# Performance work log

Hardware: AMD Instinct MI355X
Metric: run time of the kernel (lower is better)

## Reference

```python
import jax, jax.numpy as jnp
import numpy as np

N_NODES = 100000
N_EDGES = 3200000
FEAT_DIM = 128
EMBED_DIM = 128


def setup_inputs() -> dict:
    key = jax.random.key(0)
    k1, k2, k3, k4, k5 = jax.random.split(key, 5)
    x = jax.random.normal(k1, (N_NODES, FEAT_DIM), dtype=jnp.float32)
    weight = jax.random.normal(k2, (EMBED_DIM, FEAT_DIM), dtype=jnp.float32) * (1.0 / np.sqrt(FEAT_DIM))
    edge_weight = jax.random.uniform(k3, (N_EDGES,), dtype=jnp.float32)
    edge_src = jax.random.randint(k4, (N_EDGES,), 0, N_NODES, dtype=jnp.int32)
    edge_dst = jnp.sort(jax.random.randint(k5, (N_EDGES,), 0, N_NODES, dtype=jnp.int32))
    return {"x": x, "weight": weight, "edge_weight": edge_weight,
            "edge_src": edge_src, "edge_dst": edge_dst}


def reference(x, weight, edge_weight, edge_src, edge_dst):
    # Unfused GCN layer: dense transform then sparse aggregation.
    # h = X W^T  : [N, embed_dim]
    h = jnp.einsum('nf,ef->ne', x, weight)
    # out = A @ h, with A given as weighted edge list (dst <- src).
    msgs = edge_weight[:, None] * h[edge_src]          # [E, embed_dim]
    out = jax.ops.segment_sum(msgs, edge_dst, num_segments=N_NODES)
    return out
```

## Files before the change

kernel.cpp:

```cpp
#include <hip/hip_runtime.h>

#define NN 100000
#define NE 3200000
#define FEAT 128
#define EMBED 128

typedef __attribute__((ext_vector_type(8))) __bf16 bf16x8;
typedef __attribute__((ext_vector_type(8))) unsigned short ushort8;
typedef __attribute__((ext_vector_type(4))) float f32x4;

static __device__ __forceinline__ unsigned short f2bf(float f) {
    unsigned u = __float_as_uint(f);
    return (unsigned short)((u + 0x7FFFu + ((u >> 16) & 1u)) >> 16);
}

__global__ void convert_w(const float* __restrict__ w, unsigned short* __restrict__ wbf) {
    int i = blockIdx.x * 256 + threadIdx.x;
    if (i < EMBED * FEAT) wbf[i] = f2bf(w[i]);
}

__global__ __launch_bounds__(256)
void gemm_xwT(const float* __restrict__ x, const unsigned short* __restrict__ wbf,
              unsigned short* __restrict__ hbf) {
    int wave = blockIdx.x * 4 + (threadIdx.x >> 6);
    long row0 = (long)wave * 16;
    if (row0 >= NN) return;
    int lane = threadIdx.x & 63;
    int r = lane & 15, kg = lane >> 4;

    const float4* x4 = (const float4*)x;
    const bf16x8* wb = (const bf16x8*)wbf;

    bf16x8 afr[4];
#pragma unroll
    for (int ks = 0; ks < 4; ++ks) {
        long base = (row0 + r) * 32 + ks * 8 + kg * 2;
        float4 v0 = x4[base];
        float4 v1 = x4[base + 1];
        float xf[8] = {v0.x, v0.y, v0.z, v0.w, v1.x, v1.y, v1.z, v1.w};
        ushort8 au;
#pragma unroll
        for (int e = 0; e < 8; ++e) au[e] = f2bf(xf[e]);
        afr[ks] = __builtin_bit_cast(bf16x8, au);
    }

    f32x4 acc[8];
#pragma unroll
    for (int nt = 0; nt < 8; ++nt) acc[nt] = (f32x4){0.f, 0.f, 0.f, 0.f};

#pragma unroll
    for (int nt = 0; nt < 8; ++nt) {
#pragma unroll
        for (int ks = 0; ks < 4; ++ks) {
            bf16x8 b = wb[(nt * 16 + r) * 16 + ks * 4 + kg];
            acc[nt] = __builtin_amdgcn_mfma_f32_16x16x32_bf16(afr[ks], b, acc[nt], 0, 0, 0);
        }
    }

#pragma unroll
    for (int nt = 0; nt < 8; ++nt) {
#pragma unroll
        for (int reg = 0; reg < 4; ++reg) {
            hbf[(row0 + kg * 4 + reg) * 128 + nt * 16 + r] = f2bf(acc[nt][reg]);
        }
    }
}

__global__ void build_rowptr(const int* __restrict__ dst, int* __restrict__ rowptr) {
    int n = blockIdx.x * blockDim.x + threadIdx.x;
    if (n > NN) return;
    int lo = 0, hi = NE;
    while (lo < hi) {
        int mid = (lo + hi) >> 1;
        if (dst[mid] < n) lo = mid + 1; else hi = mid;
    }
    rowptr[n] = lo;
}

#define CONS(vj, wjv)                                                         \
    acc[0] += wjv * __uint_as_float(vj.x << 16);                              \
    acc[1] += wjv * __uint_as_float(vj.x & 0xFFFF0000u);                      \
    acc[2] += wjv * __uint_as_float(vj.y << 16);                              \
    acc[3] += wjv * __uint_as_float(vj.y & 0xFFFF0000u);                      \
    acc[4] += wjv * __uint_as_float(vj.z << 16);                              \
    acc[5] += wjv * __uint_as_float(vj.z & 0xFFFF0000u);                      \
    acc[6] += wjv * __uint_as_float(vj.w << 16);                              \
    acc[7] += wjv * __uint_as_float(vj.w & 0xFFFF0000u);

__global__ __launch_bounds__(256)
void aggregate(const unsigned int* __restrict__ h32, const float* __restrict__ ew,
               const int* __restrict__ src, const int* __restrict__ rowptr,
               float* __restrict__ out) {
    int wave = (int)((blockIdx.x * 256u + threadIdx.x) >> 6);
    int lane = threadIdx.x & 63;
    int nid0 = wave * 8;
    if (nid0 >= NN) return;

    int q = lane >> 4;
    int c = lane & 15;
    const uint4* h4 = (const uint4*)h32;

    int start = __builtin_amdgcn_readfirstlane(rowptr[nid0]);
    int nmax = NN - nid0 < 8 ? NN - nid0 : 8;

    for (int k = 0; k < nmax; ++k) {
        int nid = nid0 + k;
        int end = __builtin_amdgcn_readfirstlane(rowptr[nid + 1]);

        float acc[8];
#pragma unroll
        for (int j = 0; j < 8; ++j) acc[j] = 0.f;

        int i = start;
        int nfull = (end - start) >> 2;
#pragma unroll 4
        for (int b = 0; b < nfull; ++b, i += 4) {
            int s0 = src[i], s1 = src[i + 1], s2 = src[i + 2], s3 = src[i + 3];
            float w0 = ew[i], w1 = ew[i + 1], w2 = ew[i + 2], w3 = ew[i + 3];
            int   si = q == 0 ? s0 : (q == 1 ? s1 : (q == 2 ? s2 : s3));
            float wi = q == 0 ? w0 : (q == 1 ? w1 : (q == 2 ? w2 : w3));
            uint4 v = h4[(unsigned)si * 16u + (unsigned)c];
            CONS(v, wi)
        }
        if (i < end) {
            int last = end - 1;
            int i1 = i + 1 < end ? i + 1 : last;
            int i2 = i + 2 < end ? i + 2 : last;
            int s0 = src[i], s1 = src[i1], s2 = src[i2];
            float w0 = ew[i];
            float w1 = i + 1 < end ? ew[i1] : 0.f;
            float w2 = i + 2 < end ? ew[i2] : 0.f;
            int   si = q == 0 ? s0 : (q == 1 ? s1 : s2);
            float wi = q == 0 ? w0 : (q == 1 ? w1 : (q == 2 ? w2 : 0.f));
            uint4 v = h4[(unsigned)si * 16u + (unsigned)c];
            CONS(v, wi)
        }
        start = end;

#pragma unroll
        for (int j = 0; j < 8; ++j) {
            acc[j] += __shfl_xor(acc[j], 16);
            acc[j] += __shfl_xor(acc[j], 32);
        }

        if (q == 0) {
            float4* op = (float4*)(out + (long)nid * 128 + c * 8);
            op[0] = make_float4(acc[0], acc[1], acc[2], acc[3]);
            op[1] = make_float4(acc[4], acc[5], acc[6], acc[7]);
        }
    }
}

extern "C" void kernel_launch(void* const* d_in, const int* in_sizes, int n_in,
                              void* d_out, int out_size, void* d_ws, size_t ws_size,
                              hipStream_t stream) {
    const float* x    = (const float*)d_in[0];
    const float* w    = (const float*)d_in[1];
    const float* ew   = (const float*)d_in[2];
    const int*   esrc = (const int*)d_in[3];
    const int*   edst = (const int*)d_in[4];
    float* out = (float*)d_out;

    unsigned short* hbf = (unsigned short*)d_ws;
    int* rowptr = (int*)((char*)d_ws + (size_t)NN * 128 * 2);
    unsigned short* wbf = (unsigned short*)((char*)d_ws + (size_t)NN * 128 * 2 + 400016);

    convert_w<<<64, 256, 0, stream>>>(w, wbf);
    gemm_xwT<<<(NN / 16 + 3) / 4, 256, 0, stream>>>(x, wbf, hbf);
    build_rowptr<<<(NN + 1 + 255) / 256, 256, 0, stream>>>(edst, rowptr);
    aggregate<<<(NN + 31) / 32, 256, 0, stream>>>((const unsigned int*)hbf, ew, esrc, rowptr, out);
}
```

Baseline: 176.3 us.

## Split aggregation per node and column half with block swizzle across slices

The aggregate kernel now assigns one wave to a single destination node and half of the 128 embedding columns, instead of one wave serially handling 8 nodes. Each wave processes 8 edges per step with 8 lanes per edge, and block IDs are swizzled so that the two column-half blocks for the same nodes launch next to each other, which may improve L2 sharing of the gathered rows. The aim is more parallelism and less per-wave serial work and load imbalance. In exchange, src and edge weights are read twice, there are more waves and an extra shuffle stage, and the gathered row segments are 64 bytes instead of 128.

```diff
diff --git a/kernel.cpp b/kernel.cpp
--- a/kernel.cpp
+++ b/kernel.cpp
@@ -87,67 +87,80 @@
     acc[6] += wjv * __uint_as_float(vj.w << 16);                              \
     acc[7] += wjv * __uint_as_float(vj.w & 0xFFFF0000u);
 
+#define SEL8(r_, a0, a1, a2, a3, a4, a5, a6, a7)                              \
+    (q == 0 ? a0 : q == 1 ? a1 : q == 2 ? a2 : q == 3 ? a3 :                  \
+     q == 4 ? a4 : q == 5 ? a5 : q == 6 ? a6 : a7)
+
 __global__ __launch_bounds__(256)
 void aggregate(const unsigned int* __restrict__ h32, const float* __restrict__ ew,
                const int* __restrict__ src, const int* __restrict__ rowptr,
                float* __restrict__ out) {
-    int wave = (int)((blockIdx.x * 256u + threadIdx.x) >> 6);
+    unsigned bid = blockIdx.x;
+    unsigned x = bid & 7u;
+    unsigned slice = x >> 2;
+    unsigned nbIdx = (bid >> 3) * 4 + (x & 3);
+    int wid = (int)(nbIdx * 4 + (threadIdx.x >> 6));
     int lane = threadIdx.x & 63;
-    int nid0 = wave * 8;
-    if (nid0 >= NN) return;
+    if (wid >= NN) return;
+    int start = __builtin_amdgcn_readfirstlane(rowptr[wid]);
+    int end   = __builtin_amdgcn_readfirstlane(rowptr[wid + 1]);
 
-    int q = lane >> 4;
-    int c = lane & 15;
+    int q = lane >> 3;
+    int c = lane & 7;
     const uint4* h4 = (const uint4*)h32;
+    unsigned cbase = slice * 8u + (unsigned)c;
 
-    int start = __builtin_amdgcn_readfirstlane(rowptr[nid0]);
-    int nmax = NN - nid0 < 8 ? NN - nid0 : 8;
+    float acc[8];
+#pragma unroll
+    for (int j = 0; j < 8; ++j) acc[j] = 0.f;
 
-    for (int k = 0; k < nmax; ++k) {
-        int nid = nid0 + k;
-        int end = __builtin_amdgcn_readfirstlane(rowptr[nid + 1]);
-
-        float acc[8];
-#pragma unroll
-        for (int j = 0; j < 8; ++j) acc[j] = 0.f;
-
-        int i = start;
-        int nfull = (end - start) >> 2;
-#pragma unroll 4
-        for (int b = 0; b < nfull; ++b, i += 4) {
-            int s0 = src[i], s1 = src[i + 1], s2 = src[i + 2], s3 = src[i + 3];
-            float w0 = ew[i], w1 = ew[i + 1], w2 = ew[i + 2], w3 = ew[i + 3];
-            int   si = q == 0 ? s0 : (q == 1 ? s1 : (q == 2 ? s2 : s3));
-            float wi = q == 0 ? w0 : (q == 1 ? w1 : (q == 2 ? w2 : w3));
-            uint4 v = h4[(unsigned)si * 16u + (unsigned)c];
-            CONS(v, wi)
-        }
-        if (i < end) {
-            int last = end - 1;
-            int i1 = i + 1 < end ? i + 1 : last;
-            int i2 = i + 2 < end ? i + 2 : last;
-            int s0 = src[i], s1 = src[i1], s2 = src[i2];
-            float w0 = ew[i];
-            float w1 = i + 1 < end ? ew[i1] : 0.f;
-            float w2 = i + 2 < end ? ew[i2] : 0.f;
-            int   si = q == 0 ? s0 : (q == 1 ? s1 : s2);
-            float wi = q == 0 ? w0 : (q == 1 ? w1 : (q == 2 ? w2 : 0.f));
-            uint4 v = h4[(unsigned)si * 16u + (unsigned)c];
-            CONS(v, wi)
-        }
-        start = end;
+    int i = start;
+    int nfull = (end - start) >> 3;
+#pragma unroll 2
+    for (int b = 0; b < nfull; ++b, i += 8) {
+        int s0 = src[i],     s1 = src[i + 1], s2 = src[i + 2], s3 = src[i + 3];
+        int s4 = src[i + 4], s5 = src[i + 5], s6 = src[i + 6], s7 = src[i + 7];
+        float w0 = ew[i],     w1 = ew[i + 1], w2 = ew[i + 2], w3 = ew[i + 3];
+        float w4 = ew[i + 4], w5 = ew[i + 5], w6 = ew[i + 6], w7 = ew[i + 7];
+        int   si = SEL8(q, s0, s1, s2, s3, s4, s5, s6, s7);
+        float wi = SEL8(q, w0, w1, w2, w3, w4, w5, w6, w7);
+        uint4 v = h4[(unsigned)si * 16u + cbase];
+        CONS(v, wi)
+    }
+    if (i < end) {
+        int last = end - 1;
+        int e1 = i + 1 > last ? last : i + 1;
+        int e2 = i + 2 > last ? last : i + 2;
+        int e3 = i + 3 > last ? last : i + 3;
+        int e4 = i + 4 > last ? last : i + 4;
+        int e5 = i + 5 > last ? last : i + 5;
+        int e6 = i + 6 > last ? last : i + 6;
+        int s0 = src[i], s1 = src[e1], s2 = src[e2], s3 = src[e3];
+        int s4 = src[e4], s5 = src[e5], s6 = src[e6];
+        float w0 = ew[i];
+        float w1 = i + 1 < end ? ew[e1] : 0.f;
+        float w2 = i + 2 < end ? ew[e2] : 0.f;
+        float w3 = i + 3 < end ? ew[e3] : 0.f;
+        float w4 = i + 4 < end ? ew[e4] : 0.f;
+        float w5 = i + 5 < end ? ew[e5] : 0.f;
+        float w6 = i + 6 < end ? ew[e6] : 0.f;
+        int   si = SEL8(q, s0, s1, s2, s3, s4, s5, s6, s6);
+        float wi = SEL8(q, w0, w1, w2, w3, w4, w5, w6, 0.f);
+        uint4 v = h4[(unsigned)si * 16u + cbase];
+        CONS(v, wi)
+    }
 
 #pragma unroll
-        for (int j = 0; j < 8; ++j) {
-            acc[j] += __shfl_xor(acc[j], 16);
-            acc[j] += __shfl_xor(acc[j], 32);
-        }
+    for (int j = 0; j < 8; ++j) {
+        acc[j] += __shfl_xor(acc[j], 8);
+        acc[j] += __shfl_xor(acc[j], 16);
+        acc[j] += __shfl_xor(acc[j], 32);
+    }
 
-        if (q == 0) {
-            float4* op = (float4*)(out + (long)nid * 128 + c * 8);
-            op[0] = make_float4(acc[0], acc[1], acc[2], acc[3]);
-            op[1] = make_float4(acc[4], acc[5], acc[6], acc[7]);
-        }
+    if (q == 0) {
+        float4* op = (float4*)(out + (long)wid * 128 + slice * 64 + c * 8);
+        op[0] = make_float4(acc[0], acc[1], acc[2], acc[3]);
+        op[1] = make_float4(acc[4], acc[5], acc[6], acc[7]);
     }
 }
 
@@ -168,5 +181,5 @@
     convert_w<<<64, 256, 0, stream>>>(w, wbf);
     gemm_xwT<<<(NN / 16 + 3) / 4, 256, 0, stream>>>(x, wbf, hbf);
     build_rowptr<<<(NN + 1 + 255) / 256, 256, 0, stream>>>(edst, rowptr);
-    aggregate<<<(NN + 31) / 32, 256, 0, stream>>>((const unsigned int*)hbf, ew, esrc, rowptr, out);
+    aggregate<<<50000, 256, 0, stream>>>((const unsigned int*)hbf, ew, esrc, rowptr, out);
 }
```

Result: slower. 210.4 us (+19.4%).
